# Performance work log

Measured on AMD Instinct MI355X. Metric: run time of the kernel, lower is better.

Reference implementation:

```python
import jax, jax.numpy as jnp
import numpy as np

B, N, F = 4, 3000, 128

def setup_inputs() -> dict:
    key = jax.random.key(0)
    k1, k2, k3, k4 = jax.random.split(key, 4)
    x = jax.random.normal(k1, (B, N, F), dtype=jnp.float32)
    adj = jax.random.uniform(k2, (B, N, N), dtype=jnp.float32)
    h0 = jax.random.normal(k3, (B, N, F), dtype=jnp.float32)
    stdv = 1.0 / np.sqrt(F)
    theta = jax.random.uniform(k4, (F, F), dtype=jnp.float32, minval=-stdv, maxval=stdv)
    return {
        "x": x, "adj": adj, "h0": h0, "theta": theta,
        "lamda": jnp.float32(0.5), "alpha": jnp.float32(0.1), "l": 4,
    }

def _normalize_adj(adj):
    # add self loops, then D^{-1/2} A D^{-1/2} via elementwise row/col scaling
    # (same math as diag-embed + inverse + two bmms in the original)
    n = adj.shape[1]
    adj = adj + jnp.eye(n, dtype=adj.dtype)
    deg = jnp.sum(adj, axis=2)                      # [B, N]
    d_inv_sqrt = jax.lax.rsqrt(deg)                 # [B, N]
    return d_inv_sqrt[:, :, None] * adj * d_inv_sqrt[:, None, :]

def reference(x, adj, h0, theta, lamda, alpha, l):
    adj_n = _normalize_adj(adj)
    beta = jnp.log(lamda / l + 1.0)
    hi = jnp.einsum('bnm,bmf->bnf', adj_n, x)       # aggregation
    support = (1.0 - alpha) * hi + alpha * h0       # variant=False path
    r = support
    out = beta * jnp.einsum('bnf,fg->bng', support, theta) + (1.0 - beta) * r
    return out
```

## Files before the change

kernel.cpp:

```cpp
#include <hip/hip_runtime.h>
#include <hip/hip_bf16.h>
#include <math.h>

#define BB 4
#define NN 3000
#define FF 128
#define NP 3008
#define CP 3072
#define NKC 96
#define NIT 188

typedef __bf16 bf16x8 __attribute__((ext_vector_type(8)));
typedef __bf16 bf16x4 __attribute__((ext_vector_type(4)));
typedef float  f32x4  __attribute__((ext_vector_type(4)));

__global__ __launch_bounds__(256) void k_deg(const float* __restrict__ adj,
                                             __bf16* __restrict__ adjh,
                                             float* __restrict__ dis) {
    int wid  = (blockIdx.x * 256 + threadIdx.x) >> 6;
    int lane = threadIdx.x & 63;
    int b = wid / NP, i = wid % NP;
    bool rowok = i < NN;
    const float* row = adj + ((size_t)b * NN + (rowok ? i : 0)) * NN;
    __bf16* drow = adjh + (size_t)wid * CP;
    float s = 0.f;
    for (int c = lane; c < CP / 4; c += 64) {
        int col = c * 4;
        float4 v = {0.f, 0.f, 0.f, 0.f};
        if (rowok && col < NN) v = *(const float4*)(row + col);
        s += (v.x + v.y) + (v.z + v.w);
        bf16x4 h;
        h[0] = (__bf16)v.x; h[1] = (__bf16)v.y;
        h[2] = (__bf16)v.z; h[3] = (__bf16)v.w;
        *(bf16x4*)(drow + col) = h;
    }
    for (int off = 32; off > 0; off >>= 1) s += __shfl_down(s, off, 64);
    if (lane == 0 && rowok) dis[b * NN + i] = 1.0f / sqrtf(s + 1.0f);
}

__global__ __launch_bounds__(256) void k_xpk(const float* __restrict__ x,
                                             const float* __restrict__ dis,
                                             __bf16* __restrict__ xpk) {
    int b  = blockIdx.y, kc = blockIdx.x;
    int t  = threadIdx.x, w = t >> 6, l = t & 63;
    int m  = l & 15, q = l >> 4;
    #pragma unroll
    for (int h = 0; h < 2; ++h) {
        int nt = w + h * 4;
        int f  = nt * 16 + m;
        bf16x8 v;
        #pragma unroll
        for (int j = 0; j < 8; ++j) {
            int k = kc * 32 + q * 8 + j;
            float val = 0.f;
            if (k < NN) val = dis[b * NN + k] * x[((size_t)b * NN + k) * FF + f];
            v[j] = (__bf16)val;
        }
        *(bf16x8*)(xpk + ((size_t)(b * 8 + nt) * NKC + kc) * 512 + l * 8) = v;
    }
}

__global__ __launch_bounds__(256) void k_thpk(const float* __restrict__ theta,
                                              __bf16* __restrict__ thpk) {
    int kc = blockIdx.x;
    int t  = threadIdx.x, w = t >> 6, l = t & 63;
    int m  = l & 15, q = l >> 4;
    #pragma unroll
    for (int h = 0; h < 2; ++h) {
        int nt = w + h * 4;
        bf16x8 v;
        #pragma unroll
        for (int j = 0; j < 8; ++j) {
            int k = kc * 32 + q * 8 + j;
            v[j] = (__bf16)theta[k * FF + nt * 16 + m];
        }
        *(bf16x8*)(thpk + ((size_t)(nt * 4 + kc)) * 512 + l * 8) = v;
    }
}

__global__ __launch_bounds__(256) void k_agg(const __bf16* __restrict__ adjh,
                                             const __bf16* __restrict__ xpk,
                                             const __bf16* __restrict__ thpk,
                                             const float* __restrict__ x,
                                             const float* __restrict__ h0,
                                             const float* __restrict__ dis,
                                             float* __restrict__ out,
                                             const float* __restrict__ alpha_p,
                                             const float* __restrict__ lamda_p,
                                             const int* __restrict__ l_p) {
    __shared__ __bf16 tile[2][16][520];
    __shared__ __bf16 stile[16][136];
    const int b  = blockIdx.y;
    const int it = blockIdx.x;
    const int i0 = it * 16;
    const int t  = threadIdx.x, w = t >> 6, l = t & 63;
    const int m  = l & 15, quad = l >> 4;
    const int n0 = w * 32;
    const __bf16* B0 = xpk + ((size_t)(b * 8 + 2 * w) * NKC) * 512 + l * 8;
    const __bf16* B1 = B0 + (size_t)NKC * 512;
    f32x4 acc0 = {0.f, 0.f, 0.f, 0.f};
    f32x4 acc1 = {0.f, 0.f, 0.f, 0.f};

    auto issue = [&](int c, int cb) {
        #pragma unroll
        for (int i = 0; i < 4; ++i) {
            int row = i * 4 + w;
            const __bf16* g = adjh + ((size_t)(b * NP) + i0 + row) * CP + c * 512 + l * 8;
            __builtin_amdgcn_global_load_lds(
                (const __attribute__((address_space(1))) unsigned int*)g,
                (__attribute__((address_space(3))) unsigned int*)&tile[cb][row][0],
                16, 0, 0);
        }
    };

    issue(0, 0);
    __syncthreads();
    for (int c = 0; c < 6; ++c) {
        int cb = c & 1;
        if (c < 5) issue(c + 1, cb ^ 1);
        #pragma unroll 4
        for (int kcl = 0; kcl < 16; ++kcl) {
            int kc = c * 16 + kcl;
            bf16x8 a  = *(const bf16x8*)&tile[cb][m][kcl * 32 + quad * 8];
            bf16x8 b0 = *(const bf16x8*)(B0 + (size_t)kc * 512);
            bf16x8 b1 = *(const bf16x8*)(B1 + (size_t)kc * 512);
            acc0 = __builtin_amdgcn_mfma_f32_16x16x32_bf16(a, b0, acc0, 0, 0, 0);
            acc1 = __builtin_amdgcn_mfma_f32_16x16x32_bf16(a, b1, acc1, 0, 0, 0);
        }
        __syncthreads();
    }

    const float alpha = *alpha_p;
    const float beta  = logf(*lamda_p / (float)(*l_p) + 1.0f);
    float s0v[4], s1v[4];
    #pragma unroll
    for (int r = 0; r < 4; ++r) {
        int row  = quad * 4 + r;
        int irow = i0 + row;
        float s0 = 0.f, s1 = 0.f;
        if (irow < NN) {
            float  di   = dis[b * NN + irow];
            size_t base = ((size_t)b * NN + irow) * FF;
            int c0 = n0 + m, c1 = n0 + 16 + m;
            s0 = (1.f - alpha) * (di * acc0[r] + di * di * x[base + c0]) + alpha * h0[base + c0];
            s1 = (1.f - alpha) * (di * acc1[r] + di * di * x[base + c1]) + alpha * h0[base + c1];
        }
        s0v[r] = s0; s1v[r] = s1;
        stile[row][n0 + m]      = (__bf16)s0;
        stile[row][n0 + 16 + m] = (__bf16)s1;
    }
    __syncthreads();
    f32x4 o0 = {0.f, 0.f, 0.f, 0.f};
    f32x4 o1 = {0.f, 0.f, 0.f, 0.f};
    const __bf16* T0 = thpk + (size_t)(2 * w * 4) * 512 + l * 8;
    const __bf16* T1 = T0 + 4 * 512;
    #pragma unroll
    for (int kc = 0; kc < 4; ++kc) {
        bf16x8 a   = *(const bf16x8*)&stile[m][kc * 32 + quad * 8];
        bf16x8 tb0 = *(const bf16x8*)(T0 + (size_t)kc * 512);
        bf16x8 tb1 = *(const bf16x8*)(T1 + (size_t)kc * 512);
        o0 = __builtin_amdgcn_mfma_f32_16x16x32_bf16(a, tb0, o0, 0, 0, 0);
        o1 = __builtin_amdgcn_mfma_f32_16x16x32_bf16(a, tb1, o1, 0, 0, 0);
    }
    const float omb = 1.f - beta;
    #pragma unroll
    for (int r = 0; r < 4; ++r) {
        int irow = i0 + quad * 4 + r;
        if (irow < NN) {
            size_t base = ((size_t)b * NN + irow) * FF;
            out[base + n0 + m]      = beta * o0[r] + omb * s0v[r];
            out[base + n0 + 16 + m] = beta * o1[r] + omb * s1v[r];
        }
    }
}

extern "C" void kernel_launch(void* const* d_in, const int* in_sizes, int n_in,
                              void* d_out, int out_size, void* d_ws, size_t ws_size,
                              hipStream_t stream) {
    const float* x      = (const float*)d_in[0];
    const float* adj    = (const float*)d_in[1];
    const float* h0     = (const float*)d_in[2];
    const float* theta  = (const float*)d_in[3];
    const float* lamda  = (const float*)d_in[4];
    const float* alpha  = (const float*)d_in[5];
    const int*   l      = (const int*)d_in[6];
    float* out = (float*)d_out;

    char*   ws   = (char*)d_ws;
    float*  dis  = (float*)ws;
    __bf16* xpk  = (__bf16*)(ws + 65536);
    __bf16* thpk = (__bf16*)(ws + 3276800);
    __bf16* adjh = (__bf16*)(ws + 4 * 1024 * 1024);

    k_deg<<<dim3(BB * NP / 4), 256, 0, stream>>>(adj, adjh, dis);
    k_thpk<<<dim3(4), 256, 0, stream>>>(theta, thpk);
    k_xpk<<<dim3(NKC, BB), 256, 0, stream>>>(x, dis, xpk);
    k_agg<<<dim3(NIT, BB), 256, 0, stream>>>(adjh, xpk, thpk, x, h0, dis, out,
                                             alpha, lamda, l);
}
```

Measured before the change: 288.9 us.

## Load adjacency fragments directly from global memory, drop LDS double-buffering

The aggregation kernel no longer stages adjacency tiles into LDS with async global-to-LDS loads and barriers. Each lane now reads its MFMA A-fragment straight from global memory. The grid is flattened so the batch index is interleaved with the row-tile index, and the stile padding changes to 140 with 4-byte-aligned half loads. The aim is to remove LDS traffic and the per-chunk barriers, at the cost of each of the four waves re-reading the same A rows from global/L2, with no explicit prefetch.

```diff
diff --git a/kernel.cpp b/kernel.cpp
--- a/kernel.cpp
+++ b/kernel.cpp
@@ -12,6 +12,7 @@
 
 typedef __bf16 bf16x8 __attribute__((ext_vector_type(8)));
 typedef __bf16 bf16x4 __attribute__((ext_vector_type(4)));
+typedef __bf16 bf16x4a __attribute__((ext_vector_type(4), aligned(4)));
 typedef float  f32x4  __attribute__((ext_vector_type(4)));
 
 __global__ __launch_bounds__(256) void k_deg(const float* __restrict__ adj,
@@ -88,48 +89,27 @@
                                              const float* __restrict__ alpha_p,
                                              const float* __restrict__ lamda_p,
                                              const int* __restrict__ l_p) {
-    __shared__ __bf16 tile[2][16][520];
-    __shared__ __bf16 stile[16][136];
-    const int b  = blockIdx.y;
-    const int it = blockIdx.x;
+    __shared__ __bf16 stile[16][140];
+    const int id = blockIdx.x;
+    const int b  = id & 3;
+    const int it = id >> 2;
     const int i0 = it * 16;
     const int t  = threadIdx.x, w = t >> 6, l = t & 63;
     const int m  = l & 15, quad = l >> 4;
     const int n0 = w * 32;
+    const __bf16* Ap = adjh + ((size_t)(b * NP) + i0 + m) * CP + quad * 8;
     const __bf16* B0 = xpk + ((size_t)(b * 8 + 2 * w) * NKC) * 512 + l * 8;
     const __bf16* B1 = B0 + (size_t)NKC * 512;
     f32x4 acc0 = {0.f, 0.f, 0.f, 0.f};
     f32x4 acc1 = {0.f, 0.f, 0.f, 0.f};
-
-    auto issue = [&](int c, int cb) {
-        #pragma unroll
-        for (int i = 0; i < 4; ++i) {
-            int row = i * 4 + w;
-            const __bf16* g = adjh + ((size_t)(b * NP) + i0 + row) * CP + c * 512 + l * 8;
-            __builtin_amdgcn_global_load_lds(
-                (const __attribute__((address_space(1))) unsigned int*)g,
-                (__attribute__((address_space(3))) unsigned int*)&tile[cb][row][0],
-                16, 0, 0);
-        }
-    };
-
-    issue(0, 0);
-    __syncthreads();
-    for (int c = 0; c < 6; ++c) {
-        int cb = c & 1;
-        if (c < 5) issue(c + 1, cb ^ 1);
-        #pragma unroll 4
-        for (int kcl = 0; kcl < 16; ++kcl) {
-            int kc = c * 16 + kcl;
-            bf16x8 a  = *(const bf16x8*)&tile[cb][m][kcl * 32 + quad * 8];
-            bf16x8 b0 = *(const bf16x8*)(B0 + (size_t)kc * 512);
-            bf16x8 b1 = *(const bf16x8*)(B1 + (size_t)kc * 512);
-            acc0 = __builtin_amdgcn_mfma_f32_16x16x32_bf16(a, b0, acc0, 0, 0, 0);
-            acc1 = __builtin_amdgcn_mfma_f32_16x16x32_bf16(a, b1, acc1, 0, 0, 0);
-        }
-        __syncthreads();
+    #pragma unroll 4
+    for (int kc = 0; kc < NKC; ++kc) {
+        bf16x8 a  = *(const bf16x8*)(Ap + kc * 32);
+        bf16x8 b0 = *(const bf16x8*)(B0 + (size_t)kc * 512);
+        bf16x8 b1 = *(const bf16x8*)(B1 + (size_t)kc * 512);
+        acc0 = __builtin_amdgcn_mfma_f32_16x16x32_bf16(a, b0, acc0, 0, 0, 0);
+        acc1 = __builtin_amdgcn_mfma_f32_16x16x32_bf16(a, b1, acc1, 0, 0, 0);
     }
-
     const float alpha = *alpha_p;
     const float beta  = logf(*lamda_p / (float)(*l_p) + 1.0f);
     float s0v[4], s1v[4];
@@ -156,7 +136,9 @@
     const __bf16* T1 = T0 + 4 * 512;
     #pragma unroll
     for (int kc = 0; kc < 4; ++kc) {
-        bf16x8 a   = *(const bf16x8*)&stile[m][kc * 32 + quad * 8];
+        bf16x4a alo = *(const bf16x4a*)&stile[m][kc * 32 + quad * 8];
+        bf16x4a ahi = *(const bf16x4a*)&stile[m][kc * 32 + quad * 8 + 4];
+        bf16x8 a = __builtin_shufflevector(alo, ahi, 0, 1, 2, 3, 4, 5, 6, 7);
         bf16x8 tb0 = *(const bf16x8*)(T0 + (size_t)kc * 512);
         bf16x8 tb1 = *(const bf16x8*)(T1 + (size_t)kc * 512);
         o0 = __builtin_amdgcn_mfma_f32_16x16x32_bf16(a, tb0, o0, 0, 0, 0);
@@ -195,6 +177,6 @@
     k_deg<<<dim3(BB * NP / 4), 256, 0, stream>>>(adj, adjh, dis);
     k_thpk<<<dim3(4), 256, 0, stream>>>(theta, thpk);
     k_xpk<<<dim3(NKC, BB), 256, 0, stream>>>(x, dis, xpk);
-    k_agg<<<dim3(NIT, BB), 256, 0, stream>>>(adjh, xpk, thpk, x, h0, dis, out,
-                                             alpha, lamda, l);
+    k_agg<<<dim3(NIT * BB), 256, 0, stream>>>(adjh, xpk, thpk, x, h0, dis, out,
+                                              alpha, lamda, l);
 }
```

Result: slower. 307.5 us (+6.4%).
